# Optimization experiments

Measured on AMD Instinct MI355X. Metric: run time of the kernel, lower is better.

## Reference

```python
import jax, jax.numpy as jnp
import numpy as np
from jax.scipy.stats import norm
from jax.scipy.special import ndtri

B, S, F = 512, 2048, 128

def setup_inputs() -> dict:
    key = jax.random.key(0)
    k1, k2, k3 = jax.random.split(key, 3)
    x = jax.random.normal(k1, (B, F), dtype=jnp.float32)
    cdf_data = jax.random.normal(k2, (S, F), dtype=jnp.float32)
    bw_param = jax.random.uniform(k3, (1, F), dtype=jnp.float32)
    return {"x": x, "cdf_data": cdf_data, "bw_param": bw_param}

def reference(x, cdf_data, bw_param):
    # trainable bandwidths: bw = sigmoid(raw param), shape [1, F]
    bw = jax.nn.sigmoid(bw_param)[0]  # [F]
    # Pairwise Gaussian-CDF KDE: for each (b, f), mean over stored samples s of
    # Phi((x[b,f] - cdf_data[s,f]) / bw[f]).  Intermediate z: [B, S, F].
    z = (x[:, None, :] - cdf_data[None, :, :]) / bw  # [B, S, F]
    u = jnp.mean(norm.cdf(z), axis=1)               # [B, F], uniform-ish in (0,1)
    # normal_backtransform=True: map uniform -> standard normal via inverse CDF
    return ndtri(u)
```

## Files before the change

kernel.cpp:

```cpp
#include <hip/hip_runtime.h>
#include <math.h>

#define FDIM  128
#define SDIM  2048
#define BDIM  512
#define GPTS  48
#define SP    16
#define PARTS 4
#define BLOCK1 (FDIM * PARTS)
#define XMIN  (-6.0)
#define XSPAN (12.0)
#define FG    4
#define BG    64
#define BLOCK2 256
#define PERF  (SP * GPTS)

__device__ __forceinline__ double ndtri_pair(double u, double cu) {
    double q = u - 0.5;
    if (fabs(q) <= 0.425) {
        double r = 0.180625 - q * q;
        double num = (((((((2.5090809287301226727e3  * r + 3.3430575583588128105e4) * r +
                            6.7265770927008700853e4) * r + 4.5921953931549871457e4) * r +
                            1.3731693765509461125e4) * r + 1.9715909503065514427e3) * r +
                            1.3314166789178437745e2) * r + 3.3871328727963666080e0);
        double den = (((((((5.2264952788528545610e3  * r + 2.8729085735721942674e4) * r +
                            3.9307895800092710610e4) * r + 2.1213794301586595867e4) * r +
                            5.3941960214247511077e3) * r + 6.8718700749205790830e2) * r +
                            4.2313330701600911252e1) * r + 1.0);
        return q * num / den;
    }
    double r = (q < 0.0) ? u : cu;
    r = fmax(r, 1e-300);
    r = sqrt(-log(r));
    double val;
    if (r <= 5.0) {
        r -= 1.6;
        double num = (((((((7.74545014278341407640e-4 * r + 2.27238449892691845833e-2) * r +
                            2.41780725177450611770e-1) * r + 1.27045825245236838258e0) * r +
                            3.64784832476320460504e0)  * r + 5.76949722146069140550e0) * r +
                            4.63033784615654529590e0)  * r + 1.42343711074968357734e0);
        double den = (((((((1.05075007164441684324e-9 * r + 5.47593808499534494600e-4) * r +
                            1.51986665636164571966e-2) * r + 1.48103976427480074590e-1) * r +
                            6.89767334985100004550e-1) * r + 1.67638483018380384940e0) * r +
                            2.05319162663775882187e0)  * r + 1.0);
        val = num / den;
    } else {
        r -= 5.0;
        double num = (((((((2.01033439929228813265e-7 * r + 2.71155556874348757815e-5) * r +
                            1.24266094738807843860e-3) * r + 2.65321895265761230930e-2) * r +
                            2.96560571828504891230e-1) * r + 1.78482653991729133580e0) * r +
                            5.46378491116411436990e0)  * r + 6.65790464350110377720e0);
        double den = (((((((2.04426310338993978564e-15 * r + 1.42151175831644588870e-7) * r +
                            1.84631831751005468180e-5)  * r + 7.86869131145613259100e-4) * r +
                            1.48753612908506148525e-2)  * r + 1.36929880922735805310e-1) * r +
                            5.99832206555887937690e-1)  * r + 1.0);
        val = num / den;
    }
    return (q < 0.0) ? -val : val;
}

__global__ __launch_bounds__(BLOCK1) void build_kernel(
    const float* __restrict__ cdf, const float* __restrict__ bwp,
    float4* __restrict__ part4)
{
    const int g    = blockIdx.x >> 4;
    const int sp   = blockIdx.x & (SP - 1);
    const int f    = threadIdx.x & (FDIM - 1);
    const int part = threadIdx.x >> 7;

    const float p = bwp[f];
    const float s = (1.0f + __expf(-p)) * 0.70710678118654752f;
    const float c1s    = 0.3275911f * s;
    const float negs2l = -(s * s) * 1.4426950408889634f;
    const float xg = (float)(XMIN + (double)g * (XSPAN / (GPTS - 1)));

    const int chunk = SDIM / SP / PARTS;
    const int base  = sp * (SDIM / SP) + part * chunk;
    const float* cp = cdf + base * FDIM + f;

    float acc0 = 0.f, acc1 = 0.f, acc2 = 0.f, acc3 = 0.f;
    float dac = 0.f;
    int npos = 0;

    #pragma unroll 2
    for (int i = 0; i < chunk; i += 4) {
        float c0 = cp[0 * FDIM];
        float c1 = cp[1 * FDIM];
        float c2 = cp[2 * FDIM];
        float c3 = cp[3 * FDIM];
        cp += 4 * FDIM;

        float d0 = xg - c0, d1 = xg - c1, d2 = xg - c2, d3 = xg - c3;

        float t0 = __builtin_amdgcn_rcpf(fmaf(c1s, fabsf(d0), 1.0f));
        float t1 = __builtin_amdgcn_rcpf(fmaf(c1s, fabsf(d1), 1.0f));
        float t2 = __builtin_amdgcn_rcpf(fmaf(c1s, fabsf(d2), 1.0f));
        float t3 = __builtin_amdgcn_rcpf(fmaf(c1s, fabsf(d3), 1.0f));

        float x0 = exp2f(d0 * d0 * negs2l);
        float x1 = exp2f(d1 * d1 * negs2l);
        float x2 = exp2f(d2 * d2 * negs2l);
        float x3 = exp2f(d3 * d3 * negs2l);

        float q0 = fmaf(0.53070271450f, t0, -0.72657601350f);
        float q1 = fmaf(0.53070271450f, t1, -0.72657601350f);
        float q2 = fmaf(0.53070271450f, t2, -0.72657601350f);
        float q3 = fmaf(0.53070271450f, t3, -0.72657601350f);
        q0 = fmaf(q0, t0, 0.71070687050f);  q1 = fmaf(q1, t1, 0.71070687050f);
        q2 = fmaf(q2, t2, 0.71070687050f);  q3 = fmaf(q3, t3, 0.71070687050f);
        q0 = fmaf(q0, t0, -0.14224836800f); q1 = fmaf(q1, t1, -0.14224836800f);
        q2 = fmaf(q2, t2, -0.14224836800f); q3 = fmaf(q3, t3, -0.14224836800f);
        q0 = fmaf(q0, t0, 0.12741479600f);  q1 = fmaf(q1, t1, 0.12741479600f);
        q2 = fmaf(q2, t2, 0.12741479600f);  q3 = fmaf(q3, t3, 0.12741479600f);

        float e0 = q0 * t0 * x0;
        float e1 = q1 * t1 * x1;
        float e2 = q2 * t2 * x2;
        float e3 = q3 * t3 * x3;

        bool p0 = d0 >= 0.f, p1 = d1 >= 0.f, p2 = d2 >= 0.f, p3 = d3 >= 0.f;
        acc0 += p0 ? -e0 : e0;
        acc1 += p1 ? -e1 : e1;
        acc2 += p2 ? -e2 : e2;
        acc3 += p3 ? -e3 : e3;
        npos += (int)p0 + (int)p1 + (int)p2 + (int)p3;
        dac  += (x0 + x1) + (x2 + x3);
    }

    __shared__ float sacc[PARTS][FDIM];
    __shared__ float sdac[PARTS][FDIM];
    __shared__ int   snp[PARTS][FDIM];
    sacc[part][f] = (acc0 + acc1) + (acc2 + acc3);
    sdac[part][f] = dac;
    snp[part][f]  = npos;
    __syncthreads();

    if (part == 0) {
        float a  = (sacc[0][f] + sacc[1][f]) + (sacc[2][f] + sacc[3][f]);
        float da = (sdac[0][f] + sdac[1][f]) + (sdac[2][f] + sdac[3][f]);
        int   np = snp[0][f] + snp[1][f] + snp[2][f] + snp[3][f];
        part4[f * PERF + sp * GPTS + g] = make_float4(a, da, (float)np, 0.f);
    }
}

__global__ __launch_bounds__(BLOCK2) void interp_kernel(
    const float* __restrict__ x, const float* __restrict__ bwp,
    const float4* __restrict__ part4, float* __restrict__ out)
{
    const int fg = blockIdx.x & 31;
    const int bg = blockIdx.x >> 5;
    const int F0 = fg * FG;
    const int B0 = bg * BG;
    const int tid = threadIdx.x;

    __shared__ float4 sp4[FG * PERF];
    __shared__ double tab[FG * GPTS][3];

    const float4* src = part4 + (size_t)F0 * PERF;
    #pragma unroll
    for (int k = tid; k < FG * PERF; k += BLOCK2) sp4[k] = src[k];
    __syncthreads();

    if (tid < FG * GPTS) {
        const int fi = tid / GPTS;
        const int g  = tid - fi * GPTS;
        double a = 0.0, da = 0.0, np = 0.0;
        const int base = fi * PERF + g;
        #pragma unroll
        for (int sp = 0; sp < SP; ++sp) {
            float4 v = sp4[base + sp * GPTS];
            a  += (double)v.x;
            da += (double)v.y;
            np += (double)v.z;
        }
        const double invS = 1.0 / (double)SDIM;
        const double invbw = 1.0 + exp(-(double)bwp[F0 + fi]);
        tab[tid][0] = (np + a) * invS;
        tab[tid][1] = (((double)SDIM - np) - a) * invS;
        tab[tid][2] = da * invbw * (invS / 2.5066282746310002);
    }
    __syncthreads();

    const int bl = tid >> 2;
    const int fi = tid & 3;
    const int idx = (B0 + bl) * FDIM + F0 + fi;

    const double H = XSPAN / (GPTS - 1);
    double t = ((double)x[idx] - XMIN) * ((GPTS - 1) / XSPAN);
    t = fmin(fmax(t, 0.0), (double)(GPTS - 1));
    int i = (int)t;
    if (i > GPTS - 2) i = GPTS - 2;
    double w = t - (double)i;

    const int r0 = fi * GPTS + i;
    double u0 = tab[r0][0],     u1 = tab[r0 + 1][0];
    double c0 = tab[r0][1],     c1 = tab[r0 + 1][1];
    double m0 = tab[r0][2],     m1 = tab[r0 + 1][2];

    double w2 = w * w, w3 = w2 * w;
    double h00 = 2.0 * w3 - 3.0 * w2 + 1.0;
    double h10 = w3 - 2.0 * w2 + w;
    double h01 = 3.0 * w2 - 2.0 * w3;
    double h11 = w3 - w2;
    double dterm = H * (h10 * m0 + h11 * m1);
    double u  = h00 * u0 + h01 * u1 + dterm;
    double cu = h00 * c0 + h01 * c1 - dterm;

    out[idx] = (float)ndtri_pair(u, cu);
}

extern "C" void kernel_launch(void* const* d_in, const int* in_sizes, int n_in,
                              void* d_out, int out_size, void* d_ws, size_t ws_size,
                              hipStream_t stream) {
    const float* x   = (const float*)d_in[0];
    const float* cdf = (const float*)d_in[1];
    const float* bwp = (const float*)d_in[2];
    float* out = (float*)d_out;

    float4* part4 = (float4*)d_ws;

    build_kernel<<<dim3(GPTS * SP), dim3(BLOCK1), 0, stream>>>(cdf, bwp, part4);
    interp_kernel<<<dim3((FDIM / FG) * (BDIM / BG)), dim3(BLOCK2), 0, stream>>>(
        x, bwp, part4, out);
}
```

Measured before the change: 71.86 us.

## Shrink interpolation grid, rebalance build split, and fold sign count into float partials

Reduces the interpolation grid from 48 to 40 points, which cuts build work by about a sixth. The sample-space split changes from 16 to 32 chunks with 2 parts per block. The positive-sample count is folded into the float accumulator as 1-e, so partials shrink from float4 to float2, and the interp kernel now uses 2 features per block. The intent is less build compute and less partial-sum traffic. The coarser grid risks lower interpolation accuracy, and float accumulation of the 1-e terms may lose precision.

```diff
diff --git a/kernel.cpp b/kernel.cpp
--- a/kernel.cpp
+++ b/kernel.cpp
@@ -4,14 +4,14 @@
 #define FDIM  128
 #define SDIM  2048
 #define BDIM  512
-#define GPTS  48
-#define SP    16
-#define PARTS 4
+#define GPTS  40
+#define SP    32
+#define PARTS 2
 #define BLOCK1 (FDIM * PARTS)
 #define XMIN  (-6.0)
 #define XSPAN (12.0)
-#define FG    4
-#define BG    64
+#define FG    2
+#define BG    128
 #define BLOCK2 256
 #define PERF  (SP * GPTS)
 
@@ -61,9 +61,9 @@
 
 __global__ __launch_bounds__(BLOCK1) void build_kernel(
     const float* __restrict__ cdf, const float* __restrict__ bwp,
-    float4* __restrict__ part4)
+    float2* __restrict__ part2)
 {
-    const int g    = blockIdx.x >> 4;
+    const int g    = blockIdx.x >> 5;
     const int sp   = blockIdx.x & (SP - 1);
     const int f    = threadIdx.x & (FDIM - 1);
     const int part = threadIdx.x >> 7;
@@ -80,7 +80,6 @@
 
     float acc0 = 0.f, acc1 = 0.f, acc2 = 0.f, acc3 = 0.f;
     float dac = 0.f;
-    int npos = 0;
 
     #pragma unroll 2
     for (int i = 0; i < chunk; i += 4) {
@@ -118,71 +117,65 @@
         float e2 = q2 * t2 * x2;
         float e3 = q3 * t3 * x3;
 
-        bool p0 = d0 >= 0.f, p1 = d1 >= 0.f, p2 = d2 >= 0.f, p3 = d3 >= 0.f;
-        acc0 += p0 ? -e0 : e0;
-        acc1 += p1 ? -e1 : e1;
-        acc2 += p2 ? -e2 : e2;
-        acc3 += p3 ? -e3 : e3;
-        npos += (int)p0 + (int)p1 + (int)p2 + (int)p3;
+        acc0 += (d0 >= 0.f) ? (1.0f - e0) : e0;
+        acc1 += (d1 >= 0.f) ? (1.0f - e1) : e1;
+        acc2 += (d2 >= 0.f) ? (1.0f - e2) : e2;
+        acc3 += (d3 >= 0.f) ? (1.0f - e3) : e3;
         dac  += (x0 + x1) + (x2 + x3);
     }
 
     __shared__ float sacc[PARTS][FDIM];
     __shared__ float sdac[PARTS][FDIM];
-    __shared__ int   snp[PARTS][FDIM];
     sacc[part][f] = (acc0 + acc1) + (acc2 + acc3);
     sdac[part][f] = dac;
-    snp[part][f]  = npos;
     __syncthreads();
 
     if (part == 0) {
-        float a  = (sacc[0][f] + sacc[1][f]) + (sacc[2][f] + sacc[3][f]);
-        float da = (sdac[0][f] + sdac[1][f]) + (sdac[2][f] + sdac[3][f]);
-        int   np = snp[0][f] + snp[1][f] + snp[2][f] + snp[3][f];
-        part4[f * PERF + sp * GPTS + g] = make_float4(a, da, (float)np, 0.f);
+        float a  = sacc[0][f] + sacc[1][f];
+        float da = sdac[0][f] + sdac[1][f];
+        part2[f * PERF + sp * GPTS + g] = make_float2(a, da);
     }
 }
 
 __global__ __launch_bounds__(BLOCK2) void interp_kernel(
     const float* __restrict__ x, const float* __restrict__ bwp,
-    const float4* __restrict__ part4, float* __restrict__ out)
+    const float2* __restrict__ part2, float* __restrict__ out)
 {
-    const int fg = blockIdx.x & 31;
-    const int bg = blockIdx.x >> 5;
+    const int fg = blockIdx.x & 63;
+    const int bg = blockIdx.x >> 6;
     const int F0 = fg * FG;
     const int B0 = bg * BG;
     const int tid = threadIdx.x;
 
-    __shared__ float4 sp4[FG * PERF];
+    __shared__ float2 sp2[FG * PERF];
     __shared__ double tab[FG * GPTS][3];
 
-    const float4* src = part4 + (size_t)F0 * PERF;
+    const float2* src = part2 + (size_t)F0 * PERF;
     #pragma unroll
-    for (int k = tid; k < FG * PERF; k += BLOCK2) sp4[k] = src[k];
+    for (int k = tid; k < FG * PERF; k += BLOCK2) sp2[k] = src[k];
     __syncthreads();
 
     if (tid < FG * GPTS) {
         const int fi = tid / GPTS;
         const int g  = tid - fi * GPTS;
-        double a = 0.0, da = 0.0, np = 0.0;
+        double a = 0.0, da = 0.0;
         const int base = fi * PERF + g;
         #pragma unroll
         for (int sp = 0; sp < SP; ++sp) {
-            float4 v = sp4[base + sp * GPTS];
+            float2 v = sp2[base + sp * GPTS];
             a  += (double)v.x;
             da += (double)v.y;
-            np += (double)v.z;
         }
         const double invS = 1.0 / (double)SDIM;
         const double invbw = 1.0 + exp(-(double)bwp[F0 + fi]);
-        tab[tid][0] = (np + a) * invS;
-        tab[tid][1] = (((double)SDIM - np) - a) * invS;
+        tab[tid][0] = a * invS;
+        tab[tid][1] = ((double)SDIM - a) * invS;
         tab[tid][2] = da * invbw * (invS / 2.5066282746310002);
     }
     __syncthreads();
 
-    const int bl = tid >> 2;
-    const int fi = tid & 3;
+    const int bl = tid >> 1;
+    const int fi = tid & 1;
     const int idx = (B0 + bl) * FDIM + F0 + fi;
 
     const double H = XSPAN / (GPTS - 1);
@@ -193,9 +186,9 @@
     double w = t - (double)i;
 
     const int r0 = fi * GPTS + i;
-    double u0 = tab[r0][0],     u1 = tab[r0 + 1][0];
-    double c0 = tab[r0][1],     c1 = tab[r0 + 1][1];
-    double m0 = tab[r0][2],     m1 = tab[r0 + 1][2];
+    double u0 = tab[r0][0], u1 = tab[r0 + 1][0];
+    double c0 = tab[r0][1], c1 = tab[r0 + 1][1];
+    double m0 = tab[r0][2], m1 = tab[r0 + 1][2];
 
     double w2 = w * w, w3 = w2 * w;
     double h00 = 2.0 * w3 - 3.0 * w2 + 1.0;
@@ -217,9 +210,9 @@
     const float* bwp = (const float*)d_in[2];
     float* out = (float*)d_out;
 
-    float4* part4 = (float4*)d_ws;
-
-    build_kernel<<<dim3(GPTS * SP), dim3(BLOCK1), 0, stream>>>(cdf, bwp, part4);
+    float2* part2 = (float2*)d_ws;
+
+    build_kernel<<<dim3(GPTS * SP), dim3(BLOCK1), 0, stream>>>(cdf, bwp, part2);
     interp_kernel<<<dim3((FDIM / FG) * (BDIM / BG)), dim3(BLOCK2), 0, stream>>>(
-        x, bwp, part4, out);
-}
+        x, bwp, part2, out);
+}
```

After: 69.24 us. 3.6% less time.
